# Kernel optimization log

Hardware: AMD Instinct MI355X
Metric: run time of the kernel (lower is better)

The kernel has to match this reference:

```python
import jax, jax.numpy as jnp
import numpy as np

_MAX_SQRT_GRADIENT = 1000.0
NUM_HEADS = 16


@jax.custom_vjp
def sqrt_bound(x):
    return jnp.sqrt(x)

def _sb_fwd(x):
    return jnp.sqrt(x), x

def _sb_bwd(x, g):
    return (g / jnp.sqrt(jnp.clip(4.0 * x, 1.0 / _MAX_SQRT_GRADIENT**2)),)

sqrt_bound.defvjp(_sb_fwd, _sb_bwd)


def block_diag_linear(x, w):
    # x: [..., H*I], w: [H, I, J]
    H, I, J = w.shape
    xb = x.reshape(x.shape[:-1] + (H, I))
    y = jnp.einsum('bshi,hij->bshj', xb, w)
    return y.reshape(x.shape[:-1] + (H * J,))


def self_att_pool(h, num_heads):
    # h: [B, S, D]; attention over S, then max over S with keepdims
    n_state = h.shape[-1] // num_heads
    scores = jnp.matmul(h, jnp.swapaxes(h, -2, -1)) * (1.0 / np.sqrt(n_state))
    attn = jax.nn.softmax(scores, axis=-1)              # [B, S, S]
    pooled = jnp.matmul(attn, h)                        # [B, S, D]
    return jnp.max(pooled, axis=-2, keepdims=True)      # [B, 1, D]


def setup_inputs() -> dict:
    key = jax.random.key(0)
    k1, k2, k3, k4 = jax.random.split(key, 4)
    B, S, D = 4, 4096, 2048
    H = NUM_HEADS
    bw = D // H  # 128
    std = np.sqrt(1.0 / bw)
    x = jax.random.normal(k1, (B, S, D), dtype=jnp.float32)
    h = jax.random.normal(k2, (B, S, D), dtype=jnp.float32)
    w_in = jax.random.normal(k3, (H, bw, bw), dtype=jnp.float32) * std
    w_a = jax.random.normal(k4, (H, bw, bw), dtype=jnp.float32) * std
    # rnn_param_init: uniform in [min_r^2+eps, max_r^2+eps], 0.5*log, then softplus-inverse of -t
    rng = np.random.default_rng(0)
    eps = 1e-8
    u = rng.uniform(0.9**2 + eps, 0.999**2 + eps, size=(D,)).astype(np.float32)
    t = 0.5 * np.log(u)
    a_param = jnp.asarray(np.log(np.exp(-t) - 1.0).astype(np.float32))
    return {"x": x, "h": h, "w_in": w_in, "w_a": w_a, "a_param": a_param}


def reference(x, h, w_in, w_a, a_param):
    gate_x = jax.nn.sigmoid(block_diag_linear(x, w_in))
    gate_a = jax.nn.sigmoid(block_diag_linear(x, w_a))
    log_a = -8.0 * jax.nn.softplus(a_param) * gate_a     # [B, S, D]
    a = jnp.exp(log_a)
    gated_x = x * gate_x
    normalized_x = gated_x * sqrt_bound(1.0 - jnp.exp(2.0 * log_a))
    h_pooled = self_att_pool(h, NUM_HEADS)               # [B, 1, D]
    return a * h_pooled + normalized_x
```

## Files before the change

kernel.cpp:

```cpp
#include <hip/hip_runtime.h>
#include <hip/hip_bf16.h>
#include <cstdint>

typedef _Float16 f16;
typedef _Float16 f16x4 __attribute__((ext_vector_type(4)));
typedef _Float16 f16x8 __attribute__((ext_vector_type(8)));
typedef float f32x4 __attribute__((ext_vector_type(4)));

#define B_ 4
#define S_ 4096
#define D_ 2048
#define NH 16
#define BW 128

__global__ __launch_bounds__(256) void cvt_kernel(const float* __restrict__ h,
                                                  f16* __restrict__ hf,
                                                  f16* __restrict__ hT) {
    __shared__ f16 tile[64][72];
    int s0 = blockIdx.y * 64;
    int d0 = blockIdx.x * 64;
    int tid = threadIdx.x;
    int r  = tid >> 4;
    int c4 = (tid & 15) * 4;
    #pragma unroll
    for (int rr = r; rr < 64; rr += 16) {
        f32x4 v = *(const f32x4*)(h + (size_t)(s0 + rr) * D_ + d0 + c4);
        f16x4 o;
        o[0] = (f16)v[0]; o[1] = (f16)v[1]; o[2] = (f16)v[2]; o[3] = (f16)v[3];
        *(f16x4*)(hf + (size_t)(s0 + rr) * D_ + d0 + c4) = o;
        tile[rr][c4 + 0] = o[0]; tile[rr][c4 + 1] = o[1];
        tile[rr][c4 + 2] = o[2]; tile[rr][c4 + 3] = o[3];
    }
    __syncthreads();
    #pragma unroll
    for (int dd = r; dd < 64; dd += 16) {
        f16x4 o;
        o[0] = tile[c4 + 0][dd]; o[1] = tile[c4 + 1][dd];
        o[2] = tile[c4 + 2][dd]; o[3] = tile[c4 + 3][dd];
        *(f16x4*)(hT + (size_t)(d0 + dd) * S_ + s0 + c4) = o;
    }
}

__global__ __launch_bounds__(256) void prep_wT(const float* __restrict__ w,
                                               f16* __restrict__ wT) {
    int hd = blockIdx.x;
    const float* src = w + hd * 16384;
    f16* dst = wT + hd * 16384;
    int tid = threadIdx.x;
    int j0 = (tid & 31) * 4;
    #pragma unroll
    for (int p = 0; p < 16; p++) {
        int i = (tid >> 5) + p * 8;
        f32x4 v = *(const f32x4*)(src + i * 128 + j0);
        int kc = i >> 5, il = i & 31;
        #pragma unroll
        for (int e = 0; e < 4; e++)
            dst[kc * 4096 + (j0 + e) * 32 + il] = (f16)v[e];
    }
}

__device__ __forceinline__ unsigned f2ord(float f) {
    unsigned u = __float_as_uint(f);
    return (u & 0x80000000u) ? ~u : (u | 0x80000000u);
}

template<int EPI>
__global__ __launch_bounds__(256) void gemm_nt(const f16* __restrict__ A,
                                               const f16* __restrict__ Bm,
                                               void* __restrict__ C,
                                               unsigned* __restrict__ hp,
                                               int M, int N, int K, float alpha) {
    __shared__ f16 lA[128 * 32];
    __shared__ f16 lB[128 * 32];
    int tid  = threadIdx.x;
    int m0   = blockIdx.y * 128;
    int n0   = blockIdx.x * 128;
    int wave = tid >> 6;
    int lane = tid & 63;
    int wr   = (wave >> 1) * 64;
    int wc   = (wave & 1) * 64;
    int l15  = lane & 15;
    int quad = lane >> 4;

    const f16* aSrc = A + (size_t)(m0 + (tid >> 2)) * K + (tid & 3) * 8;
    const f16* bSrc = Bm + (size_t)(n0 + (tid >> 2)) * K + (tid & 3) * 8;
    size_t rowStep = (size_t)64 * K;

    f32x4 acc[4][4];
    #pragma unroll
    for (int i = 0; i < 4; i++)
        #pragma unroll
        for (int j = 0; j < 4; j++) acc[i][j] = (f32x4)0.0f;

    for (int k0 = 0; k0 < K; k0 += 32) {
        __builtin_amdgcn_global_load_lds(
            (const __attribute__((address_space(1))) void*)(aSrc),
            (__attribute__((address_space(3))) void*)(lA + tid * 8), 16, 0, 0);
        __builtin_amdgcn_global_load_lds(
            (const __attribute__((address_space(1))) void*)(aSrc + rowStep),
            (__attribute__((address_space(3))) void*)(lA + 2048 + tid * 8), 16, 0, 0);
        __builtin_amdgcn_global_load_lds(
            (const __attribute__((address_space(1))) void*)(bSrc),
            (__attribute__((address_space(3))) void*)(lB + tid * 8), 16, 0, 0);
        __builtin_amdgcn_global_load_lds(
            (const __attribute__((address_space(1))) void*)(bSrc + rowStep),
            (__attribute__((address_space(3))) void*)(lB + 2048 + tid * 8), 16, 0, 0);
        __syncthreads();

        f16x8 af[4], bf[4];
        #pragma unroll
        for (int i = 0; i < 4; i++) {
            af[i] = *(const f16x8*)(lA + (wr + i * 16 + l15) * 32 + quad * 8);
            bf[i] = *(const f16x8*)(lB + (wc + i * 16 + l15) * 32 + quad * 8);
        }
        #pragma unroll
        for (int i = 0; i < 4; i++)
            #pragma unroll
            for (int j = 0; j < 4; j++)
                acc[i][j] = __builtin_amdgcn_mfma_f32_16x16x32_f16(af[i], bf[j], acc[i][j], 0, 0, 0);
        __syncthreads();
        aSrc += 32; bSrc += 32;
    }

    if (EPI == 0) {
        f16* Cf = (f16*)C;
        #pragma unroll
        for (int i = 0; i < 4; i++) {
            int row = m0 + wr + i * 16 + quad * 4;
            #pragma unroll
            for (int j = 0; j < 4; j++) {
                int col = n0 + wc + j * 16 + l15;
                f16* cp = Cf + (size_t)row * N + col;
                #pragma unroll
                for (int r = 0; r < 4; r++) cp[(size_t)r * N] = (f16)(alpha * acc[i][j][r]);
            }
        }
    } else {
        #pragma unroll
        for (int j = 0; j < 4; j++) {
            int col = n0 + wc + j * 16 + l15;
            float m = acc[0][j][0];
            #pragma unroll
            for (int i = 0; i < 4; i++)
                #pragma unroll
                for (int r = 0; r < 4; r++) m = fmaxf(m, acc[i][j][r]);
            atomicMax(hp + col, f2ord(m));
        }
    }
}

__global__ __launch_bounds__(256) void softmax_kernel(const f16* __restrict__ scores,
                                                      f16* __restrict__ attn) {
    int row = blockIdx.x;
    int tid = threadIdx.x;
    const f16* src = scores + (size_t)row * S_;
    float v[16];
    #pragma unroll
    for (int j = 0; j < 2; j++) {
        f16x8 raw = *(const f16x8*)(src + tid * 8 + j * 2048);
        #pragma unroll
        for (int e = 0; e < 8; e++) v[j * 8 + e] = (float)raw[e];
    }
    float m = -3.4e38f;
    #pragma unroll
    for (int e = 0; e < 16; e++) m = fmaxf(m, v[e]);
    #pragma unroll
    for (int o = 32; o > 0; o >>= 1) m = fmaxf(m, __shfl_xor(m, o, 64));
    __shared__ float sm[4];
    __shared__ float ss[4];
    int wave = tid >> 6, lane = tid & 63;
    if (lane == 0) sm[wave] = m;
    __syncthreads();
    m = fmaxf(fmaxf(sm[0], sm[1]), fmaxf(sm[2], sm[3]));
    float sum = 0.f;
    #pragma unroll
    for (int e = 0; e < 16; e++) { v[e] = __expf(v[e] - m); sum += v[e]; }
    #pragma unroll
    for (int o = 32; o > 0; o >>= 1) sum += __shfl_xor(sum, o, 64);
    if (lane == 0) ss[wave] = sum;
    __syncthreads();
    sum = ss[0] + ss[1] + ss[2] + ss[3];
    float inv = 1.0f / sum;
    f16* dst = attn + (size_t)row * S_;
    #pragma unroll
    for (int j = 0; j < 2; j++) {
        f16x8 o;
        #pragma unroll
        for (int e = 0; e < 8; e++) o[e] = (f16)(v[j * 8 + e] * inv);
        *(f16x8*)(dst + tid * 8 + j * 2048) = o;
    }
}

__global__ __launch_bounds__(512, 1) void final2_kernel(
    const float* __restrict__ x, const f16* __restrict__ wTi,
    const f16* __restrict__ wTa, const float* __restrict__ a_param,
    const unsigned* __restrict__ hp_u, float* __restrict__ out) {
    __shared__ f16 xs[4 * 256 * 32];
    __shared__ f16 lwi[16384];
    __shared__ f16 lwa[16384];
    int tid  = threadIdx.x;
    int hd   = blockIdx.y;
    int row0 = blockIdx.x * 256;
    int b    = row0 >> 12;
    int wave = tid >> 6, lane = tid & 63;

    const f16* wsi = wTi + hd * 16384;
    const f16* wsa = wTa + hd * 16384;
    #pragma unroll
    for (int c = 0; c < 4; c++) {
        int off = (wave * 4 + c) * 512 + lane * 8;
        __builtin_amdgcn_global_load_lds(
            (const __attribute__((address_space(1))) void*)(wsi + off),
            (__attribute__((address_space(3))) void*)(lwi + off), 16, 0, 0);
        __builtin_amdgcn_global_load_lds(
            (const __attribute__((address_space(1))) void*)(wsa + off),
            (__attribute__((address_space(3))) void*)(lwa + off), 16, 0, 0);
    }

    {
        int rr   = tid >> 4;
        int col8 = (tid & 15) * 8;
        int kc = col8 >> 5, cl = col8 & 31;
        const float* xb = x + (size_t)row0 * D_ + hd * 128;
        #pragma unroll
        for (int it = 0; it < 8; it++) {
            int row = it * 32 + rr;
            f32x4 v0 = *(const f32x4*)(xb + (size_t)row * D_ + col8);
            f32x4 v1 = *(const f32x4*)(xb + (size_t)row * D_ + col8 + 4);
            f16x8 o;
            o[0] = (f16)v0[0]; o[1] = (f16)v0[1]; o[2] = (f16)v0[2]; o[3] = (f16)v0[3];
            o[4] = (f16)v1[0]; o[5] = (f16)v1[1]; o[6] = (f16)v1[2]; o[7] = (f16)v1[3];
            *(f16x8*)(xs + kc * 8192 + row * 32 + cl) = o;
        }
    }
    __syncthreads();

    int wr = (wave >> 1) * 64;
    int wc = (wave & 1) * 64;
    int l15 = lane & 15, quad = lane >> 4;

    f32x4 ai[4][4], aa[4][4];
    #pragma unroll
    for (int i = 0; i < 4; i++)
        #pragma unroll
        for (int j = 0; j < 4; j++) { ai[i][j] = (f32x4)0.0f; aa[i][j] = (f32x4)0.0f; }

    #pragma unroll
    for (int ks = 0; ks < 4; ks++) {
        f16x8 af[4], bi[4], ba[4];
        #pragma unroll
        for (int i = 0; i < 4; i++)
            af[i] = *(const f16x8*)(xs + ks * 8192 + (wr + i * 16 + l15) * 32 + quad * 8);
        #pragma unroll
        for (int j = 0; j < 4; j++) {
            bi[j] = *(const f16x8*)(lwi + ks * 4096 + (wc + j * 16 + l15) * 32 + quad * 8);
            ba[j] = *(const f16x8*)(lwa + ks * 4096 + (wc + j * 16 + l15) * 32 + quad * 8);
        }
        #pragma unroll
        for (int i = 0; i < 4; i++)
            #pragma unroll
            for (int j = 0; j < 4; j++) {
                ai[i][j] = __builtin_amdgcn_mfma_f32_16x16x32_f16(af[i], bi[j], ai[i][j], 0, 0, 0);
                aa[i][j] = __builtin_amdgcn_mfma_f32_16x16x32_f16(af[i], ba[j], aa[i][j], 0, 0, 0);
            }
    }

    #pragma unroll
    for (int j = 0; j < 4; j++) {
        int n = wc + j * 16 + l15;
        int d = hd * 128 + n;
        float n8sp = -8.f * log1pf(__expf(a_param[d]));
        unsigned u = hp_u[b * D_ + d];
        unsigned bits = (u >> 31) ? (u ^ 0x80000000u) : ~u;
        float hpv = __uint_as_float(bits);
        int xc = (n >> 5) * 8192 + (n & 31);
        #pragma unroll
        for (int i = 0; i < 4; i++) {
            int mbase = wr + i * 16 + quad * 4;
            #pragma unroll
            for (int r = 0; r < 4; r++) {
                int m = mbase + r;
                float gx = 1.f / (1.f + __expf(-ai[i][j][r]));
                float ga = 1.f / (1.f + __expf(-aa[i][j][r]));
                float a  = __expf(n8sp * ga);
                float ns = sqrtf(fmaxf(1.f - a * a, 0.f));
                float xv = (float)xs[xc + m * 32];
                out[(size_t)(row0 + m) * D_ + d] = a * hpv + xv * gx * ns;
            }
        }
    }
}

extern "C" void kernel_launch(void* const* d_in, const int* in_sizes, int n_in,
                              void* d_out, int out_size, void* d_ws, size_t ws_size,
                              hipStream_t stream) {
    const float* x       = (const float*)d_in[0];
    const float* h       = (const float*)d_in[1];
    const float* w_in    = (const float*)d_in[2];
    const float* w_a     = (const float*)d_in[3];
    const float* a_param = (const float*)d_in[4];
    float* out = (float*)d_out;

    char* ws = (char*)d_ws;
    f16*      hf     = (f16*)ws;
    f16*      hT     = (f16*)(ws + ((size_t)16 << 20));
    f16*      scores = (f16*)(ws + ((size_t)32 << 20));
    f16*      attn   = (f16*)(ws + ((size_t)64 << 20));
    unsigned* hp     = (unsigned*)(ws + ((size_t)96 << 20));
    f16*      wTi    = (f16*)(ws + ((size_t)96 << 20) + (64 << 10));
    f16*      wTa    = (f16*)(ws + ((size_t)96 << 20) + (64 << 10) + (512 << 10));

    hipMemsetAsync(hp, 0, (size_t)B_ * D_ * sizeof(unsigned), stream);
    prep_wT<<<dim3(16), 256, 0, stream>>>(w_in, wTi);
    prep_wT<<<dim3(16), 256, 0, stream>>>(w_a, wTa);

    const float scale = 0.08838834764831845f;
    for (int b = 0; b < B_; b++) {
        const float* hb = h + (size_t)b * S_ * D_;
        cvt_kernel<<<dim3(D_ / 64, S_ / 64), 256, 0, stream>>>(hb, hf, hT);
        gemm_nt<0><<<dim3(S_ / 128, S_ / 128), 256, 0, stream>>>(
            hf, hf, (void*)scores, nullptr, S_, S_, D_, scale);
        softmax_kernel<<<dim3(S_), 256, 0, stream>>>(scores, attn);
        gemm_nt<1><<<dim3(D_ / 128, S_ / 128), 256, 0, stream>>>(
            attn, hT, nullptr, hp + b * D_, S_, D_, S_, 1.0f);
    }
    final2_kernel<<<dim3((B_ * S_) / 256, NH), 512, 0, stream>>>(
        x, wTi, wTa, a_param, hp, out);
}
```

Before: 1.400 ms.

## Exploit score symmetry in QK^T GEMM and restructure gated final kernel

The h·h^T score GEMM now computes only upper-triangular 128x128 tiles (528 blocks instead of 1024) and mirrors each off-diagonal tile into the transposed position. The final gate kernel is rewritten to use smaller 32-row tiles without LDS staging, reading weights and x directly from global memory with vectorized stores and higher occupancy. The softplus term is precomputed once in a tiny kernel. Trade-offs: the transposed writes are scattered 8-byte stores, and the final kernel re-reads weights from cache for every block.

```diff
diff --git a/kernel.cpp b/kernel.cpp
--- a/kernel.cpp
+++ b/kernel.cpp
@@ -59,17 +59,108 @@
     }
 }
 
+__global__ __launch_bounds__(256) void prep_nsp(const float* __restrict__ ap,
+                                                float* __restrict__ nsp) {
+    int d = blockIdx.x * 256 + threadIdx.x;
+    nsp[d] = -8.f * log1pf(__expf(ap[d]));
+}
+
 __device__ __forceinline__ unsigned f2ord(float f) {
     unsigned u = __float_as_uint(f);
     return (u & 0x80000000u) ? ~u : (u | 0x80000000u);
 }
 
-template<int EPI>
-__global__ __launch_bounds__(256) void gemm_nt(const f16* __restrict__ A,
-                                               const f16* __restrict__ Bm,
-                                               void* __restrict__ C,
-                                               unsigned* __restrict__ hp,
-                                               int M, int N, int K, float alpha) {
+__global__ __launch_bounds__(256) void gemm_sym(const f16* __restrict__ A,
+                                                f16* __restrict__ C,
+                                                int K, float alpha) {
+    __shared__ f16 lA[128 * 32];
+    __shared__ f16 lB[128 * 32];
+    int idx = blockIdx.x;
+    int bn = (int)((sqrtf(8.f * (float)idx + 1.f) - 1.f) * 0.5f);
+    while ((bn + 1) * (bn + 2) / 2 <= idx) bn++;
+    while (bn * (bn + 1) / 2 > idx) bn--;
+    int bm = idx - bn * (bn + 1) / 2;
+    int m0 = bm * 128, n0 = bn * 128;
+
+    int tid  = threadIdx.x;
+    int wave = tid >> 6;
+    int lane = tid & 63;
+    int wr   = (wave >> 1) * 64;
+    int wc   = (wave & 1) * 64;
+    int l15  = lane & 15;
+    int quad = lane >> 4;
+
+    const f16* aSrc = A + (size_t)(m0 + (tid >> 2)) * K + (tid & 3) * 8;
+    const f16* bSrc = A + (size_t)(n0 + (tid >> 2)) * K + (tid & 3) * 8;
+    size_t rowStep = (size_t)64 * K;
+
+    f32x4 acc[4][4];
+    #pragma unroll
+    for (int i = 0; i < 4; i++)
+        #pragma unroll
+        for (int j = 0; j < 4; j++) acc[i][j] = (f32x4)0.0f;
+
+    for (int k0 = 0; k0 < K; k0 += 32) {
+        __builtin_amdgcn_global_load_lds(
+            (const __attribute__((address_space(1))) void*)(aSrc),
+            (__attribute__((address_space(3))) void*)(lA + tid * 8), 16, 0, 0);
+        __builtin_amdgcn_global_load_lds(
+            (const __attribute__((address_space(1))) void*)(aSrc + rowStep),
+            (__attribute__((address_space(3))) void*)(lA + 2048 + tid * 8), 16, 0, 0);
+        __builtin_amdgcn_global_load_lds(
+            (const __attribute__((address_space(1))) void*)(bSrc),
+            (__attribute__((address_space(3))) void*)(lB + tid * 8), 16, 0, 0);
+        __builtin_amdgcn_global_load_lds(
+            (const __attribute__((address_space(1))) void*)(bSrc + rowStep),
+            (__attribute__((address_space(3))) void*)(lB + 2048 + tid * 8), 16, 0, 0);
+        __syncthreads();
+
+        f16x8 af[4], bf[4];
+        #pragma unroll
+        for (int i = 0; i < 4; i++) {
+            af[i] = *(const f16x8*)(lA + (wr + i * 16 + l15) * 32 + quad * 8);
+            bf[i] = *(const f16x8*)(lB + (wc + i * 16 + l15) * 32 + quad * 8);
+        }
+        #pragma unroll
+        for (int i = 0; i < 4; i++)
+            #pragma unroll
+            for (int j = 0; j < 4; j++)
+                acc[i][j] = __builtin_amdgcn_mfma_f32_16x16x32_f16(af[i], bf[j], acc[i][j], 0, 0, 0);
+        __syncthreads();
+        aSrc += 32; bSrc += 32;
+    }
+
+    #pragma unroll
+    for (int i = 0; i < 4; i++) {
+        int row = m0 + wr + i * 16 + quad * 4;
+        #pragma unroll
+        for (int j = 0; j < 4; j++) {
+            int col = n0 + wc + j * 16 + l15;
+            f16* cp = C + (size_t)row * S_ + col;
+            #pragma unroll
+            for (int r = 0; r < 4; r++) cp[(size_t)r * S_] = (f16)(alpha * acc[i][j][r]);
+        }
+    }
+    if (bm != bn) {
+        #pragma unroll
+        for (int i = 0; i < 4; i++) {
+            int colb = m0 + wr + i * 16 + quad * 4;
+            #pragma unroll
+            for (int j = 0; j < 4; j++) {
+                int row = n0 + wc + j * 16 + l15;
+                f16x4 o;
+                #pragma unroll
+                for (int r = 0; r < 4; r++) o[r] = (f16)(alpha * acc[i][j][r]);
+                *(f16x4*)(C + (size_t)row * S_ + colb) = o;
+            }
+        }
+    }
+}
+
+__global__ __launch_bounds__(256) void gemm_nt_max(const f16* __restrict__ A,
+                                                   const f16* __restrict__ Bm,
+                                                   unsigned* __restrict__ hp,
+                                                   int N, int K) {
     __shared__ f16 lA[128 * 32];
     __shared__ f16 lB[128 * 32];
     int tid  = threadIdx.x;
@@ -122,30 +213,15 @@
         aSrc += 32; bSrc += 32;
     }
 
-    if (EPI == 0) {
-        f16* Cf = (f16*)C;
-        #pragma unroll
-        for (int i = 0; i < 4; i++) {
-            int row = m0 + wr + i * 16 + quad * 4;
-            #pragma unroll
-            for (int j = 0; j < 4; j++) {
-                int col = n0 + wc + j * 16 + l15;
-                f16* cp = Cf + (size_t)row * N + col;
-                #pragma unroll
-                for (int r = 0; r < 4; r++) cp[(size_t)r * N] = (f16)(alpha * acc[i][j][r]);
-            }
-        }
-    } else {
-        #pragma unroll
-        for (int j = 0; j < 4; j++) {
-            int col = n0 + wc + j * 16 + l15;
-            float m = acc[0][j][0];
-            #pragma unroll
-            for (int i = 0; i < 4; i++)
-                #pragma unroll
-                for (int r = 0; r < 4; r++) m = fmaxf(m, acc[i][j][r]);
-            atomicMax(hp + col, f2ord(m));
-        }
+    #pragma unroll
+    for (int j = 0; j < 4; j++) {
+        int col = n0 + wc + j * 16 + l15;
+        float m = acc[0][j][0];
+        #pragma unroll
+        for (int i = 0; i < 4; i++)
+            #pragma unroll
+            for (int r = 0; r < 4; r++) m = fmaxf(m, acc[i][j][r]);
+        atomicMax(hp + col, f2ord(m));
     }
 }
 
@@ -191,102 +267,83 @@
     }
 }
 
-__global__ __launch_bounds__(512, 1) void final2_kernel(
+__global__ __launch_bounds__(256, 4) void final3_kernel(
     const float* __restrict__ x, const f16* __restrict__ wTi,
-    const f16* __restrict__ wTa, const float* __restrict__ a_param,
+    const f16* __restrict__ wTa, const float* __restrict__ nsp_arr,
     const unsigned* __restrict__ hp_u, float* __restrict__ out) {
-    __shared__ f16 xs[4 * 256 * 32];
-    __shared__ f16 lwi[16384];
-    __shared__ f16 lwa[16384];
     int tid  = threadIdx.x;
     int hd   = blockIdx.y;
-    int row0 = blockIdx.x * 256;
+    int row0 = blockIdx.x * 32;
     int b    = row0 >> 12;
     int wave = tid >> 6, lane = tid & 63;
-
-    const f16* wsi = wTi + hd * 16384;
-    const f16* wsa = wTa + hd * 16384;
-    #pragma unroll
-    for (int c = 0; c < 4; c++) {
-        int off = (wave * 4 + c) * 512 + lane * 8;
-        __builtin_amdgcn_global_load_lds(
-            (const __attribute__((address_space(1))) void*)(wsi + off),
-            (__attribute__((address_space(3))) void*)(lwi + off), 16, 0, 0);
-        __builtin_amdgcn_global_load_lds(
-            (const __attribute__((address_space(1))) void*)(wsa + off),
-            (__attribute__((address_space(3))) void*)(lwa + off), 16, 0, 0);
-    }
-
-    {
-        int rr   = tid >> 4;
-        int col8 = (tid & 15) * 8;
-        int kc = col8 >> 5, cl = col8 & 31;
-        const float* xb = x + (size_t)row0 * D_ + hd * 128;
-        #pragma unroll
-        for (int it = 0; it < 8; it++) {
-            int row = it * 32 + rr;
-            f32x4 v0 = *(const f32x4*)(xb + (size_t)row * D_ + col8);
-            f32x4 v1 = *(const f32x4*)(xb + (size_t)row * D_ + col8 + 4);
+    int l15  = lane & 15, quad = lane >> 4;
+    int jbase = wave * 32;
+
+    const f16* wi = wTi + hd * 16384;
+    const f16* wa = wTa + hd * 16384;
+    const float* xb = x + (size_t)row0 * D_ + hd * 128;
+
+    f32x4 accx[2][2], acca[2][2];
+    #pragma unroll
+    for (int im = 0; im < 2; im++)
+        #pragma unroll
+        for (int jn = 0; jn < 2; jn++) { accx[im][jn] = (f32x4)0.0f; acca[im][jn] = (f32x4)0.0f; }
+
+    #pragma unroll
+    for (int ks = 0; ks < 4; ks++) {
+        f16x8 bf[2];
+        #pragma unroll
+        for (int jn = 0; jn < 2; jn++) {
+            const float* p = xb + (size_t)(jn * 16 + l15) * D_ + ks * 32 + quad * 8;
+            f32x4 v0 = *(const f32x4*)p;
+            f32x4 v1 = *(const f32x4*)(p + 4);
             f16x8 o;
             o[0] = (f16)v0[0]; o[1] = (f16)v0[1]; o[2] = (f16)v0[2]; o[3] = (f16)v0[3];
             o[4] = (f16)v1[0]; o[5] = (f16)v1[1]; o[6] = (f16)v1[2]; o[7] = (f16)v1[3];
-            *(f16x8*)(xs + kc * 8192 + row * 32 + cl) = o;
-        }
-    }
-    __syncthreads();
-
-    int wr = (wave >> 1) * 64;
-    int wc = (wave & 1) * 64;
-    int l15 = lane & 15, quad = lane >> 4;
-
-    f32x4 ai[4][4], aa[4][4];
-    #pragma unroll
-    for (int i = 0; i < 4; i++)
-        #pragma unroll
-        for (int j = 0; j < 4; j++) { ai[i][j] = (f32x4)0.0f; aa[i][j] = (f32x4)0.0f; }
-
-    #pragma unroll
-    for (int ks = 0; ks < 4; ks++) {
-        f16x8 af[4], bi[4], ba[4];
-        #pragma unroll
-        for (int i = 0; i < 4; i++)
-            af[i] = *(const f16x8*)(xs + ks * 8192 + (wr + i * 16 + l15) * 32 + quad * 8);
-        #pragma unroll
-        for (int j = 0; j < 4; j++) {
-            bi[j] = *(const f16x8*)(lwi + ks * 4096 + (wc + j * 16 + l15) * 32 + quad * 8);
-            ba[j] = *(const f16x8*)(lwa + ks * 4096 + (wc + j * 16 + l15) * 32 + quad * 8);
-        }
-        #pragma unroll
-        for (int i = 0; i < 4; i++)
-            #pragma unroll
-            for (int j = 0; j < 4; j++) {
-                ai[i][j] = __builtin_amdgcn_mfma_f32_16x16x32_f16(af[i], bi[j], ai[i][j], 0, 0, 0);
-                aa[i][j] = __builtin_amdgcn_mfma_f32_16x16x32_f16(af[i], ba[j], aa[i][j], 0, 0, 0);
+            bf[jn] = o;
+        }
+        #pragma unroll
+        for (int im = 0; im < 2; im++) {
+            int joff = (jbase + im * 16 + l15) * 32 + quad * 8;
+            f16x8 afx = *(const f16x8*)(wi + ks * 4096 + joff);
+            f16x8 afa = *(const f16x8*)(wa + ks * 4096 + joff);
+            #pragma unroll
+            for (int jn = 0; jn < 2; jn++) {
+                accx[im][jn] = __builtin_amdgcn_mfma_f32_16x16x32_f16(afx, bf[jn], accx[im][jn], 0, 0, 0);
+                acca[im][jn] = __builtin_amdgcn_mfma_f32_16x16x32_f16(afa, bf[jn], acca[im][jn], 0, 0, 0);
             }
-    }
-
-    #pragma unroll
-    for (int j = 0; j < 4; j++) {
-        int n = wc + j * 16 + l15;
-        int d = hd * 128 + n;
-        float n8sp = -8.f * log1pf(__expf(a_param[d]));
-        unsigned u = hp_u[b * D_ + d];
-        unsigned bits = (u >> 31) ? (u ^ 0x80000000u) : ~u;
-        float hpv = __uint_as_float(bits);
-        int xc = (n >> 5) * 8192 + (n & 31);
-        #pragma unroll
-        for (int i = 0; i < 4; i++) {
-            int mbase = wr + i * 16 + quad * 4;
+        }
+    }
+
+    #pragma unroll
+    for (int im = 0; im < 2; im++) {
+        int dl = hd * 128 + jbase + im * 16 + quad * 4;
+        f32x4 nsp = *(const f32x4*)(nsp_arr + dl);
+        uint4 hu = *(const uint4*)(hp_u + b * D_ + dl);
+        float hpv[4];
+        {
+            unsigned uu[4] = {hu.x, hu.y, hu.z, hu.w};
             #pragma unroll
             for (int r = 0; r < 4; r++) {
-                int m = mbase + r;
-                float gx = 1.f / (1.f + __expf(-ai[i][j][r]));
-                float ga = 1.f / (1.f + __expf(-aa[i][j][r]));
-                float a  = __expf(n8sp * ga);
+                unsigned u = uu[r];
+                unsigned bits = (u >> 31) ? (u ^ 0x80000000u) : ~u;
+                hpv[r] = __uint_as_float(bits);
+            }
+        }
+        #pragma unroll
+        for (int jn = 0; jn < 2; jn++) {
+            int row = row0 + jn * 16 + l15;
+            f32x4 xv = *(const f32x4*)(x + (size_t)row * D_ + dl);
+            f32x4 o;
+            #pragma unroll
+            for (int r = 0; r < 4; r++) {
+                float gx = 1.f / (1.f + __expf(-accx[im][jn][r]));
+                float ga = 1.f / (1.f + __expf(-acca[im][jn][r]));
+                float a  = __expf(nsp[r] * ga);
                 float ns = sqrtf(fmaxf(1.f - a * a, 0.f));
-                float xv = (float)xs[xc + m * 32];
-                out[(size_t)(row0 + m) * D_ + d] = a * hpv + xv * gx * ns;
+                o[r] = a * hpv[r] + xv[r] * gx * ns;
             }
+            *(f32x4*)(out + (size_t)row * D_ + dl) = o;
         }
     }
 }
@@ -309,21 +366,22 @@
     unsigned* hp     = (unsigned*)(ws + ((size_t)96 << 20));
     f16*      wTi    = (f16*)(ws + ((size_t)96 << 20) + (64 << 10));
     f16*      wTa    = (f16*)(ws + ((size_t)96 << 20) + (64 << 10) + (512 << 10));
+    float*    nsp    = (float*)(ws + ((size_t)96 << 20) + (64 << 10) + (1024 << 10));
 
     hipMemsetAsync(hp, 0, (size_t)B_ * D_ * sizeof(unsigned), stream);
     prep_wT<<<dim3(16), 256, 0, stream>>>(w_in, wTi);
     prep_wT<<<dim3(16), 256, 0, stream>>>(w_a, wTa);
+    prep_nsp<<<dim3(8), 256, 0, stream>>>(a_param, nsp);
 
     const float scale = 0.08838834764831845f;
     for (int b = 0; b < B_; b++) {
         const float* hb = h + (size_t)b * S_ * D_;
         cvt_kernel<<<dim3(D_ / 64, S_ / 64), 256, 0, stream>>>(hb, hf, hT);
-        gemm_nt<0><<<dim3(S_ / 128, S_ / 128), 256, 0, stream>>>(
-            hf, hf, (void*)scores, nullptr, S_, S_, D_, scale);
+        gemm_sym<<<dim3(528), 256, 0, stream>>>(hf, scores, D_, scale);
         softmax_kernel<<<dim3(S_), 256, 0, stream>>>(scores, attn);
-        gemm_nt<1><<<dim3(D_ / 128, S_ / 128), 256, 0, stream>>>(
-            attn, hT, nullptr, hp + b * D_, S_, D_, S_, 1.0f);
-    }
-    final2_kernel<<<dim3((B_ * S_) / 256, NH), 512, 0, stream>>>(
-        x, wTi, wTa, a_param, hp, out);
-}
+        gemm_nt_max<<<dim3(D_ / 128, S_ / 128), 256, 0, stream>>>(
+            attn, hT, hp + b * D_, D_, S_);
+    }
+    final3_kernel<<<dim3((B_ * S_) / 32, NH), 256, 0, stream>>>(
+        x, wTi, wTa, nsp, hp, out);
+}
```

Result: faster. 1.255 ms (-10.4%).
